# Kernel optimization log

Measured on AMD Instinct MI355X. Metric: run time of the kernel, lower is better.

Reference implementation:

```python
import jax, jax.numpy as jnp
import numpy as np

B, S, D, H, HD = 8, 1024, 1152, 16, 72
L, R = 32, 36  # get_decompose_dim(1152)
W_BITS, A_BITS = 4, 8


def _ste_round(x):
    return x + jax.lax.stop_gradient(jnp.round(x) - x)


def _fake_quant(x, bits):
    # symmetric fake quant, per last-dim group (per-token for acts, per-out-channel for weights)
    qmax = 2.0 ** (bits - 1) - 1.0
    scale = jnp.maximum(jnp.max(jnp.abs(x), axis=-1, keepdims=True) / qmax, 1e-8)
    return jnp.clip(_ste_round(x / scale), -qmax - 1.0, qmax) * scale


def _kron_apply(x, A, Bm):
    # DecomposeTransMatrix: x (..., L*R) -> reshape (L,R), Y = A^T X B (row-vector kron transform)
    sh = x.shape
    y = jnp.einsum('...lr,lp,rq->...pq', x.reshape(sh[:-1] + (L, R)), A, Bm)
    return y.reshape(sh)


def setup_inputs() -> dict:
    key = jax.random.key(0)
    ks = jax.random.split(key, 16)
    lin = lambda k, sh: jax.random.normal(k, sh, jnp.float32) * 0.02
    return {
        'hidden_states': jax.random.normal(ks[0], (B, S, D), jnp.float32),
        'Wq': lin(ks[1], (D, D)), 'bq': lin(ks[2], (D,)),
        'Wk': lin(ks[3], (D, D)), 'bk': lin(ks[4], (D,)),
        'Wv': lin(ks[5], (D, D)), 'bv': lin(ks[6], (D,)),
        'Wo': lin(ks[7], (D, D)), 'bo': lin(ks[8], (D,)),
        'ln_A': jnp.eye(L, dtype=jnp.float32) + 0.02 * jax.random.normal(ks[9], (L, L), jnp.float32),
        'ln_B': jnp.eye(R, dtype=jnp.float32) + 0.02 * jax.random.normal(ks[10], (R, R), jnp.float32),
        'ln_diag': 1.0 + 0.1 * jax.random.uniform(ks[11], (D,), jnp.float32),
        'vc': jnp.eye(HD, dtype=jnp.float32) + 0.02 * jax.random.normal(ks[12], (HD, HD), jnp.float32),
        'o_mat': jnp.eye(H, dtype=jnp.float32) + 0.02 * jax.random.normal(ks[13], (H, H), jnp.float32),
    }


def reference(hidden_states, Wq, bq, Wk, bk, Wv, bv, Wo, bo, ln_A, ln_B, ln_diag, vc, o_mat):
    invA_T = jnp.linalg.inv(ln_A).T
    invB_T = jnp.linalg.inv(ln_B).T
    # ln_trans applied to activations (diag scale + decomposed Kronecker rotation)
    x = _kron_apply(hidden_states * ln_diag, ln_A, ln_B)  # (B,S,D)

    def qlinear(xin, W, b, out_vc=None):
        # qa_trans inv_t folded into weight: W' = kron(W/diag, invA.T, invB.T) over input dim
        Wt = _kron_apply(W * (1.0 / ln_diag), invA_T, invB_T)
        bt = b
        if out_vc is not None:  # vc_trans folded into to_v output channels
            Wt = jnp.einsum('hdi,de->hei', Wt.reshape(H, HD, D), out_vc).reshape(D, D)
            bt = (b.reshape(H, HD) @ out_vc).reshape(-1)
        return _fake_quant(xin, A_BITS) @ _fake_quant(Wt, W_BITS).T + bt

    q = qlinear(x, Wq, bq).reshape(B, S, H, HD).transpose(0, 2, 1, 3)  # (B,H,S,HD)
    k = qlinear(x, Wk, bk).reshape(B, S, H, HD).transpose(0, 2, 1, 3)
    v = qlinear(x, Wv, bv, out_vc=vc).reshape(B, S, H, HD).transpose(0, 2, 1, 3)

    # baddbmm with beta=0, alpha=1: NO 1/sqrt(d) scaling (faithful to source)
    scores = jnp.einsum('bhqd,bhkd->bhqk', q, k)
    attn = jax.nn.softmax(scores.astype(jnp.float32), axis=-1).astype(q.dtype)
    ctx = jnp.einsum('bhqk,bhkd->bhqd', attn, v).transpose(0, 2, 1, 3)  # (B,S,H,HD)

    # o_trans: matmul(o_mat.T, Y) per token
    ctx = jnp.einsum('bsgd,gh->bshd', ctx, o_mat).reshape(B, S, D)

    # to_out with qa_trans=[inv(O).T, inv(V).T] folded into weight
    o_it = jnp.linalg.inv(o_mat).T
    v_it = jnp.linalg.inv(vc).T
    Wot = jnp.einsum('gh,ogd,de->ohe', o_it, Wo.reshape(D, H, HD), v_it).reshape(D, D)
    out = _fake_quant(ctx, A_BITS) @ _fake_quant(Wot, W_BITS).T + bo
    return out  # rescale_output_factor = 1.0
```

## Files before the change

kernel.cpp:

```cpp
#include <hip/hip_runtime.h>
#include <hip/hip_bf16.h>

#define BB 8
#define SS 1024
#define DD 1152
#define HH 16
#define HD 72
#define PD 96
#define LL 32
#define RR 36
#define NTOK (BB*SS)

typedef __attribute__((ext_vector_type(8)))  short short8;
typedef __attribute__((ext_vector_type(4)))  float f32x4;
typedef __attribute__((ext_vector_type(16))) float f32x16;
typedef __attribute__((ext_vector_type(4)))  unsigned short ushort4v;

#define F_IAT   0
#define F_IBT   1024
#define F_IO    2320
#define F_IV    2576
#define F_BVT   7760
#define F_SX    16384
#define F_SWQ   24576
#define F_SWK   25728
#define F_SWV   26880
#define F_SWO   28032
#define F_SCTX  32768
#define B_R1    1048576ULL
#define B_WB    (B_R1 + 37748736ULL)
#define B_XB    (B_WB + 4ULL*2654208ULL)
#define B_QB    (B_XB + 18874368ULL)
#define B_KB    (B_QB + 25165824ULL)
#define B_VB    (B_KB + 25165824ULL)
#define B_VT    (B_VB + 25165824ULL)
#define WSLOT   1327104ULL

__device__ __forceinline__ unsigned bf16rne(float f) {
    unsigned u = __builtin_bit_cast(unsigned, f);
    return (u + 0x7fffu + ((u >> 16) & 1u)) >> 16;
}
__device__ __forceinline__ unsigned cvtpk(float lo, float hi) {
    unsigned r;
    asm("v_cvt_pk_bf16_f32 %0, %1, %2" : "=v"(r) : "v"(lo), "v"(hi));
    return r;
}
__device__ __forceinline__ short8 mk8(unsigned a, unsigned b, unsigned c, unsigned d) {
    union { unsigned u[4]; short8 s; } t;
    t.u[0] = a; t.u[1] = b; t.u[2] = c; t.u[3] = d;
    return t.s;
}
__device__ __forceinline__ void async_ld16(void* lds, const void* g) {
    __builtin_amdgcn_global_load_lds((const __attribute__((address_space(1))) unsigned*)g,
                                     (__attribute__((address_space(3))) unsigned*)lds, 16, 0, 0);
}

__global__ __launch_bounds__(128) void invert_kernel(const float* __restrict__ A32, const float* __restrict__ B36,
                                                     const float* __restrict__ O16, const float* __restrict__ V72,
                                                     float* __restrict__ ws)
{
    __shared__ float As[80*76], Xs[80*76], Ys[80*76], Ps[80*76], Wt[80*76];
    int which = blockIdx.x;
    int n; const float* src;
    if (which == 0)      { n = 32; src = A32; }
    else if (which == 1) { n = 36; src = B36; }
    else if (which == 2) { n = 16; src = O16; }
    else                 { n = 72; src = V72; }
    int tid = threadIdx.x;
    int nq = n >> 2;
    for (int idx = tid; idx < n*n; idx += 128) {
        int i = idx / n, j = idx % n;
        float a = src[idx];
        As[i*76 + j] = a;
        Xs[i*76 + j] = (i == j ? 2.0f : 0.0f) - a;
    }
    __syncthreads();
    int ty = tid >> 3, qq = tid & 7;

#define NSGEMM(DST, SA, SB) { \
    f32x4 c00={0,0,0,0},c01={0,0,0,0},c02={0,0,0,0}, \
          c10={0,0,0,0},c11={0,0,0,0},c12={0,0,0,0}, \
          c20={0,0,0,0},c21={0,0,0,0},c22={0,0,0,0}, \
          c30={0,0,0,0},c31={0,0,0,0},c32={0,0,0,0}, \
          c40={0,0,0,0},c41={0,0,0,0},c42={0,0,0,0}; \
    _Pragma("unroll 2") \
    for (int k = 0; k < n; ++k) { \
        const float* sb = &SB[k*76]; \
        f32x4 b0 = *(const f32x4*)(sb + 4*qq); \
        f32x4 b1 = *(const f32x4*)(sb + 4*qq + 32); \
        f32x4 b2 = *(const f32x4*)(sb + 4*qq + 64); \
        float a0 = SA[ty*76 + k]; \
        float a1 = SA[(ty+16)*76 + k]; \
        float a2 = SA[(ty+32)*76 + k]; \
        float a3 = SA[(ty+48)*76 + k]; \
        float a4 = SA[(ty+64)*76 + k]; \
        c00 += a0*b0; c01 += a0*b1; c02 += a0*b2; \
        c10 += a1*b0; c11 += a1*b1; c12 += a1*b2; \
        c20 += a2*b0; c21 += a2*b1; c22 += a2*b2; \
        c30 += a3*b0; c31 += a3*b1; c32 += a3*b2; \
        c40 += a4*b0; c41 += a4*b1; c42 += a4*b2; \
    } \
    { \
        f32x4 cc[5][3] = {{c00,c01,c02},{c10,c11,c12},{c20,c21,c22},{c30,c31,c32},{c40,c41,c42}}; \
        _Pragma("unroll") \
        for (int m = 0; m < 5; ++m) { \
            int i = ty + 16*m; \
            if (i < n) { \
                _Pragma("unroll") \
                for (int c = 0; c < 3; ++c) { \
                    int q = qq + 8*c; \
                    if (q < nq) *(f32x4*)&DST[i*76 + 4*q] = cc[m][c]; \
                } \
            } \
        } \
    } \
}

#define NSELEM(PD_, YD_) { \
    for (int idx = tid; idx < n*n; idx += 128) { \
        int i = idx / n, j = idx % n; \
        PD_[i*76 + j] = PD_[i*76 + j] - 3.0f*YD_[i*76 + j] + (i == j ? 3.0f : 0.0f); \
    } \
}
    NSGEMM(Ys, As, Xs); __syncthreads();
    NSGEMM(Ps, Ys, Ys); __syncthreads();
    NSELEM(Ps, Ys);     __syncthreads();
    NSGEMM(Wt, Xs, Ps); __syncthreads();
    NSGEMM(Ys, As, Wt); __syncthreads();
    NSGEMM(Ps, Ys, Ys); __syncthreads();
    NSELEM(Ps, Ys);     __syncthreads();
    NSGEMM(Xs, Wt, Ps); __syncthreads();
#undef NSGEMM
#undef NSELEM

    if (which == 0) {
        for (int idx = tid; idx < 32*32; idx += 128) { int l = idx/32, pp = idx%32; ws[F_IAT + idx] = Xs[pp*76 + l]; }
    } else if (which == 1) {
        for (int idx = tid; idx < 36*36; idx += 128) { int r = idx/36, qx = idx%36; ws[F_IBT + idx] = Xs[qx*76 + r]; }
    } else if (which == 2) {
        for (int idx = tid; idx < 16*16; idx += 128) { int i = idx/16, j = idx%16; ws[F_IO + idx] = Xs[i*76 + j]; }
    } else {
        for (int idx = tid; idx < 72*72; idx += 128) { int i = idx/72, j = idx%72; ws[F_IV + idx] = Xs[i*76 + j]; }
    }
}

__global__ __launch_bounds__(256) void kron_act_q(const float* __restrict__ src, unsigned short* __restrict__ dst,
                                                  float* __restrict__ scl,
                                                  const float* __restrict__ P, const float* __restrict__ Q,
                                                  const float* __restrict__ diag)
{
    __shared__ float Xs[LL*RR], T1[LL*RR], Ps[LL*LL], Qs[RR*RR], Ys[LL*RR], red[256];
    int row = blockIdx.x;
    int tid = threadIdx.x;
    const float* sr = src + (size_t)row*DD;
    for (int i = tid; i < LL*LL; i += 256) Ps[i] = P[i];
    for (int i = tid; i < RR*RR; i += 256) Qs[i] = Q[i];
    for (int i = tid; i < DD; i += 256) Xs[i] = sr[i]*diag[i];
    __syncthreads();
    for (int s = tid; s < 288; s += 256) {
        int p = s / 9, r4 = (s % 9)*4;
        f32x4 acc = {0.f,0.f,0.f,0.f};
        #pragma unroll 8
        for (int l = 0; l < LL; ++l) {
            float a = Ps[l*LL + p];
            f32x4 x = *(const f32x4*)&Xs[l*RR + r4];
            acc += a*x;
        }
        *(f32x4*)&T1[p*RR + r4] = acc;
    }
    __syncthreads();
    float lmax = 0.f;
    for (int s = tid; s < 288; s += 256) {
        int p = s / 9, q4 = (s % 9)*4;
        f32x4 acc = {0.f,0.f,0.f,0.f};
        #pragma unroll 9
        for (int r = 0; r < RR; ++r) {
            float t = T1[p*RR + r];
            f32x4 qv = *(const f32x4*)&Qs[r*RR + q4];
            acc += t*qv;
        }
        *(f32x4*)&Ys[p*RR + q4] = acc;
        lmax = fmaxf(lmax, fmaxf(fmaxf(fabsf(acc[0]), fabsf(acc[1])), fmaxf(fabsf(acc[2]), fabsf(acc[3]))));
    }
    red[tid] = lmax; __syncthreads();
    for (int s = 128; s > 0; s >>= 1) { if (tid < s) red[tid] = fmaxf(red[tid], red[tid+s]); __syncthreads(); }
    float scale = fmaxf(red[0]/127.f, 1e-8f);
    float rs = 1.f/scale;
    if (tid == 0) scl[row] = scale;
    for (int s = tid; s < 288; s += 256) {
        int i4 = s*4;
        f32x4 y = *(const f32x4*)&Ys[i4];
        ushort4v o;
        #pragma unroll
        for (int c = 0; c < 4; ++c) {
            float v = rintf(y[c]*rs);
            v = fminf(fmaxf(v, -128.f), 127.f);
            o[c] = (unsigned short)bf16rne(v);
        }
        *(ushort4v*)&dst[(size_t)row*DD + i4] = o;
    }
}

__global__ __launch_bounds__(256) void kron_w_q(const float* __restrict__ src, unsigned short* __restrict__ dst,
                                                float* __restrict__ scl,
                                                const float* __restrict__ P, const float* __restrict__ Q,
                                                const float* __restrict__ diag)
{
    __shared__ float Xs[LL*RR], T1[LL*RR], Ps[LL*LL], Qs[RR*RR], Ys[LL*RR], red[256];
    int row = blockIdx.x;
    int tid = threadIdx.x;
    const float* sr = src + (size_t)row*DD;
    for (int i = tid; i < LL*LL; i += 256) Ps[i] = P[i];
    for (int i = tid; i < RR*RR; i += 256) Qs[i] = Q[i];
    for (int i = tid; i < DD; i += 256) Xs[i] = sr[i]*(1.0f/diag[i]);
    __syncthreads();
    for (int s = tid; s < 288; s += 256) {
        int p = s / 9, r4 = (s % 9)*4;
        f32x4 acc = {0.f,0.f,0.f,0.f};
        #pragma unroll 8
        for (int l = 0; l < LL; ++l) {
            float a = Ps[l*LL + p];
            f32x4 x = *(const f32x4*)&Xs[l*RR + r4];
            acc += a*x;
        }
        *(f32x4*)&T1[p*RR + r4] = acc;
    }
    __syncthreads();
    float lmax = 0.f;
    for (int s = tid; s < 288; s += 256) {
        int p = s / 9, q4 = (s % 9)*4;
        f32x4 acc = {0.f,0.f,0.f,0.f};
        #pragma unroll 9
        for (int r = 0; r < RR; ++r) {
            float t = T1[p*RR + r];
            f32x4 qv = *(const f32x4*)&Qs[r*RR + q4];
            acc += t*qv;
        }
        *(f32x4*)&Ys[p*RR + q4] = acc;
        lmax = fmaxf(lmax, fmaxf(fmaxf(fabsf(acc[0]), fabsf(acc[1])), fmaxf(fabsf(acc[2]), fabsf(acc[3]))));
    }
    red[tid] = lmax; __syncthreads();
    for (int s = 128; s > 0; s >>= 1) { if (tid < s) red[tid] = fmaxf(red[tid], red[tid+s]); __syncthreads(); }
    float scale = fmaxf(red[0]/7.f, 1e-8f);
    float rs = 1.f/scale;
    if (tid == 0) scl[row] = scale;
    for (int s = tid; s < 288; s += 256) {
        int i4 = s*4;
        f32x4 y = *(const f32x4*)&Ys[i4];
        ushort4v o;
        #pragma unroll
        for (int c = 0; c < 4; ++c) {
            float v = rintf(y[c]*rs);
            v = fminf(fmaxf(v, -8.f), 7.f);
            o[c] = (unsigned short)bf16rne(v);
        }
        *(ushort4v*)&dst[(size_t)row*DD + i4] = o;
    }
}

__global__ __launch_bounds__(256) void kron_rows(const float* __restrict__ src, float* __restrict__ dst,
                                                 const float* __restrict__ P, const float* __restrict__ Q,
                                                 const float* __restrict__ diag)
{
    __shared__ float Xs[LL*RR], T1[LL*RR], Ps[LL*LL], Qs[RR*RR];
    int row = blockIdx.x;
    int tid = threadIdx.x;
    const float* sr = src + (size_t)row*DD;
    for (int i = tid; i < LL*LL; i += 256) Ps[i] = P[i];
    for (int i = tid; i < RR*RR; i += 256) Qs[i] = Q[i];
    for (int i = tid; i < DD; i += 256) Xs[i] = sr[i]*(1.0f/diag[i]);
    __syncthreads();
    for (int s = tid; s < 288; s += 256) {
        int p = s / 9, r4 = (s % 9)*4;
        f32x4 acc = {0.f,0.f,0.f,0.f};
        #pragma unroll 8
        for (int l = 0; l < LL; ++l) {
            float a = Ps[l*LL + p];
            f32x4 x = *(const f32x4*)&Xs[l*RR + r4];
            acc += a*x;
        }
        *(f32x4*)&T1[p*RR + r4] = acc;
    }
    __syncthreads();
    for (int s = tid; s < 288; s += 256) {
        int p = s / 9, q4 = (s % 9)*4;
        f32x4 acc = {0.f,0.f,0.f,0.f};
        #pragma unroll 9
        for (int r = 0; r < RR; ++r) {
            float t = T1[p*RR + r];
            f32x4 qv = *(const f32x4*)&Qs[r*RR + q4];
            acc += t*qv;
        }
        *(f32x4*)&dst[(size_t)row*DD + p*RR + q4] = acc;
    }
}

__global__ __launch_bounds__(256) void wv_fold_q(const float* __restrict__ tmp, const float* __restrict__ vc,
                                                 const float* __restrict__ bv, unsigned short* __restrict__ dst,
                                                 float* __restrict__ scl, float* __restrict__ bvt)
{
    int he = blockIdx.x;
    int h = he / HD, e = he % HD;
    __shared__ float vcol[HD], Ys[DD], red[256];
    int tid = threadIdx.x;
    if (tid < HD) vcol[tid] = vc[tid*HD + e];
    __syncthreads();
    const float* base = tmp + (size_t)h*HD*DD;
    float lmax = 0.f;
    for (int i = tid; i < DD; i += 256) {
        float acc = 0.f;
        #pragma unroll 8
        for (int d = 0; d < HD; ++d) acc += base[(size_t)d*DD + i]*vcol[d];
        Ys[i] = acc;
        lmax = fmaxf(lmax, fabsf(acc));
    }
    red[tid] = lmax; __syncthreads();
    for (int s = 128; s > 0; s >>= 1) { if (tid < s) red[tid] = fmaxf(red[tid], red[tid+s]); __syncthreads(); }
    float scale = fmaxf(red[0]/7.f, 1e-8f);
    float rs = 1.f/scale;
    if (tid == 0) {
        scl[he] = scale;
        float acc = 0.f;
        for (int d = 0; d < HD; ++d) acc += bv[h*HD + d]*vcol[d];
        bvt[he] = acc;
    }
    for (int i = tid; i < DD; i += 256) {
        float v = rintf(Ys[i]*rs);
        v = fminf(fmaxf(v, -8.f), 7.f);
        dst[(size_t)he*DD + i] = (unsigned short)bf16rne(v);
    }
}

__global__ __launch_bounds__(256) void wo_trans_q(const float* __restrict__ Wo, const float* __restrict__ iO,
                                                  const float* __restrict__ iV, unsigned short* __restrict__ dst,
                                                  float* __restrict__ scl)
{
    __shared__ float M[HH*HD], T1[HH*HD], iOs[HH*HH], iVs[HD*HD], Ys[DD], red[256];
    int row = blockIdx.x, tid = threadIdx.x;
    for (int i = tid; i < DD; i += 256) M[i] = Wo[(size_t)row*DD + i];
    for (int i = tid; i < HH*HH; i += 256) iOs[i] = iO[i];
    for (int i = tid; i < HD*HD; i += 256) iVs[i] = iV[i];
    __syncthreads();
    for (int i = tid; i < DD; i += 256) {
        int h = i / HD, d = i % HD;
        float a = 0.f;
        #pragma unroll
        for (int g = 0; g < HH; ++g) a += iOs[h*HH + g]*M[g*HD + d];
        T1[i] = a;
    }
    __syncthreads();
    float lmax = 0.f;
    for (int i = tid; i < DD; i += 256) {
        int h = i / HD, e = i % HD;
        float a = 0.f;
        #pragma unroll 8
        for (int d = 0; d < HD; ++d) a += T1[h*HD + d]*iVs[e*HD + d];
        Ys[i] = a;
        lmax = fmaxf(lmax, fabsf(a));
    }
    red[tid] = lmax; __syncthreads();
    for (int s = 128; s > 0; s >>= 1) { if (tid < s) red[tid] = fmaxf(red[tid], red[tid+s]); __syncthreads(); }
    float scale = fmaxf(red[0]/7.f, 1e-8f);
    float rs = 1.f/scale;
    if (tid == 0) scl[row] = scale;
    for (int i = tid; i < DD; i += 256) {
        float v = rintf(Ys[i]*rs);
        v = fminf(fmaxf(v, -8.f), 7.f);
        dst[(size_t)row*DD + i] = (unsigned short)bf16rne(v);
    }
}

__device__ __forceinline__ void gemm_body(const unsigned short* __restrict__ Xb, const unsigned short* __restrict__ Wb,
                                          unsigned short* As, unsigned short* Bs, f32x4 (&acc)[4][4],
                                          int wr, int wc, int lr, int lg)
{
    for (int k0 = 0; k0 < DD; k0 += 32) {
        int tid = threadIdx.x;
        #pragma unroll
        for (int j = 0; j < 2; ++j) {
            int idx = tid + j*256;
            int row = idx >> 2, pp = idx & 3;
            int s = pp ^ ((row >> 1) & 3);
            async_ld16(&As[idx*8], Xb + (size_t)row*DD + k0 + s*8);
            async_ld16(&Bs[idx*8], Wb + (size_t)row*DD + k0 + s*8);
        }
        __syncthreads();
        short8 a[4], bfr[4];
        #pragma unroll
        for (int fr = 0; fr < 4; ++fr) {
            int row = wr*64 + fr*16 + lr;
            a[fr] = *(const short8*)(&As[row*32 + (lg ^ ((row>>1)&3))*8]);
        }
        #pragma unroll
        for (int fc = 0; fc < 4; ++fc) {
            int row = wc*64 + fc*16 + lr;
            bfr[fc] = *(const short8*)(&Bs[row*32 + (lg ^ ((row>>1)&3))*8]);
        }
        #pragma unroll
        for (int fr = 0; fr < 4; ++fr)
            #pragma unroll
            for (int fc = 0; fc < 4; ++fc)
                acc[fr][fc] = __builtin_amdgcn_mfma_f32_16x16x32_bf16(a[fr], bfr[fc], acc[fr][fc], 0, 0, 0);
        __syncthreads();
    }
}

__global__ __launch_bounds__(256) void gemm_qkv(const unsigned short* __restrict__ X,
                                                const unsigned short* __restrict__ Wq_b,
                                                const unsigned short* __restrict__ Wk_b,
                                                const unsigned short* __restrict__ Wv_b,
                                                const float* __restrict__ sx, const float* __restrict__ ws_all,
                                                const float* __restrict__ bq, const float* __restrict__ bk,
                                                const float* __restrict__ bvt,
                                                unsigned short* __restrict__ qb, unsigned short* __restrict__ kb,
                                                unsigned short* __restrict__ vb)
{
    __shared__ unsigned short As[128*32];
    __shared__ unsigned short Bs[128*32];
    int bn = blockIdx.x, bm = blockIdx.y, z = blockIdx.z;
    const unsigned short* W = (z == 0) ? Wq_b : (z == 1) ? Wk_b : Wv_b;
    const float* sw_ = ws_all + (size_t)z*1152;
    const float* bias = (z == 0) ? bq : (z == 1) ? bk : bvt;
    unsigned short* outQ = (z == 0) ? qb : (z == 1) ? kb : vb;
    int tid = threadIdx.x;
    if (bn == 0 && z <= 1) {
        short8 zero = {0,0,0,0,0,0,0,0};
        for (int t = tid; t < 6144; t += 256) {
            int tok = t / 48, rem = t % 48;
            int h = rem / 3, c = rem % 3;
            int mrow = bm*128 + tok;
            int b = mrow >> 10, s = mrow & 1023;
            *(short8*)(&outQ[(((size_t)b*HH + h)*SS + s)*PD + 72 + c*8]) = zero;
        }
    }
    int wave = tid >> 6, lane = tid & 63;
    int wr = wave >> 1, wc = wave & 1;
    int lr = lane & 15, lg = lane >> 4;
    f32x4 acc[4][4];
    #pragma unroll
    for (int i = 0; i < 4; ++i)
        #pragma unroll
        for (int j = 0; j < 4; ++j)
            #pragma unroll
            for (int e = 0; e < 4; ++e) acc[i][j][e] = 0.f;
    gemm_body(X + (size_t)bm*128*DD, W + (size_t)bn*128*DD, As, Bs, acc, wr, wc, lr, lg);
    #pragma unroll
    for (int fc = 0; fc < 4; ++fc) {
        int n = bn*128 + wc*64 + fc*16 + lr;
        float swn = sw_[n], bnv = bias[n];
        int h = n/72, hd = n - (n/72)*72;
        #pragma unroll
        for (int fr = 0; fr < 4; ++fr) {
            #pragma unroll
            for (int j = 0; j < 4; ++j) {
                int mrow = bm*128 + wr*64 + fr*16 + lg*4 + j;
                float v = acc[fr][fc][j]*sx[mrow]*swn + bnv;
                int b = mrow >> 10, s = mrow & 1023;
                outQ[(((size_t)b*HH + h)*SS + s)*PD + hd] = (unsigned short)bf16rne(v);
            }
        }
    }
}

__global__ __launch_bounds__(256) void gemm_out(const unsigned short* __restrict__ X, const unsigned short* __restrict__ W,
                                                const float* __restrict__ sx, const float* __restrict__ sw_,
                                                const float* __restrict__ bias, float* __restrict__ outF)
{
    __shared__ unsigned short As[128*32];
    __shared__ unsigned short Bs[128*32];
    int bn = blockIdx.x, bm = blockIdx.y;
    int tid = threadIdx.x;
    int wave = tid >> 6, lane = tid & 63;
    int wr = wave >> 1, wc = wave & 1;
    int lr = lane & 15, lg = lane >> 4;
    f32x4 acc[4][4];
    #pragma unroll
    for (int i = 0; i < 4; ++i)
        #pragma unroll
        for (int j = 0; j < 4; ++j)
            #pragma unroll
            for (int e = 0; e < 4; ++e) acc[i][j][e] = 0.f;
    gemm_body(X + (size_t)bm*128*DD, W + (size_t)bn*128*DD, As, Bs, acc, wr, wc, lr, lg);
    #pragma unroll
    for (int fc = 0; fc < 4; ++fc) {
        int n = bn*128 + wc*64 + fc*16 + lr;
        float swn = sw_[n], bnv = bias[n];
        #pragma unroll
        for (int fr = 0; fr < 4; ++fr) {
            #pragma unroll
            for (int j = 0; j < 4; ++j) {
                int mrow = bm*128 + wr*64 + fr*16 + lg*4 + j;
                outF[(size_t)mrow*DD + n] = acc[fr][fc][j]*sx[mrow]*swn + bnv;
            }
        }
    }
}

__global__ __launch_bounds__(256) void transpose_v(const unsigned short* __restrict__ v, unsigned short* __restrict__ vT)
{
    __shared__ unsigned short t[64][100];
    int head = blockIdx.x >> 4, st = blockIdx.x & 15;
    int tid = threadIdx.x;
    const unsigned short* src = v + ((size_t)head*SS + st*64)*PD;
    for (int idx = tid; idx < 64*PD; idx += 256) {
        int i = idx / PD, d = idx % PD;
        t[i][d] = src[idx];
    }
    __syncthreads();
    unsigned short* dst = vT + (size_t)head*PD*SS + st*64;
    for (int idx = tid; idx < PD*64; idx += 256) {
        int d = idx >> 6, i = idx & 63;
        dst[(size_t)d*SS + i] = t[i][d];
    }
}

__global__ __launch_bounds__(256) void attn_mfma(const unsigned short* __restrict__ q, const unsigned short* __restrict__ k,
                                                 const unsigned short* __restrict__ vT, float* __restrict__ ctx)
{
    __shared__ unsigned short Kl[64*128];
    __shared__ unsigned short Vl[96*64];
    int blk = blockIdx.x;
    int bh = blk >> 3;
    int qblk = blk & 7;
    int tid = threadIdx.x;
    int wave = tid >> 6, lane = tid & 63;
    int lq = lane & 31, half = lane >> 5;
    int b = bh >> 4, h = bh & 15;
    const unsigned short* qbase = q + ((size_t)bh*SS + qblk*128 + wave*32)*PD;
    const unsigned short* kbase = k + (size_t)bh*SS*PD;
    const unsigned short* vtb   = vT + (size_t)bh*PD*SS;
    short8 qf[6];
    #pragma unroll
    for (int ks = 0; ks < 6; ++ks)
        qf[ks] = *(const short8*)(qbase + (size_t)lq*PD + ks*16 + half*8);
    f32x16 O0, O1, O2;
    #pragma unroll
    for (int r = 0; r < 16; ++r) { O0[r] = 0.f; O1[r] = 0.f; O2[r] = 0.f; }
    float m = -1e30f, l = 0.f;
    for (int t0 = 0; t0 < SS; t0 += 64) {
        __syncthreads();
        #pragma unroll
        for (int j = 0; j < 3; ++j) {
            int idx = tid + j*256;
            int row = idx / 12, s = idx % 12;
            int phys = s ^ (row & 7);
            short8 val = *(const short8*)(kbase + (size_t)(t0 + row)*PD + s*8);
            *(short8*)(&Kl[row*128 + phys*8]) = val;
        }
        #pragma unroll
        for (int j = 0; j < 3; ++j) {
            int idx = tid + j*256;
            int d = idx >> 3, p = idx & 7;
            int s = p ^ (d & 7);
            short8 val = *(const short8*)(vtb + (size_t)d*SS + t0 + s*8);
            *(short8*)(&Vl[d*64 + p*8]) = val;
        }
        __syncthreads();
        #pragma unroll
        for (int sub = 0; sub < 2; ++sub) {
            f32x16 sacc;
            #pragma unroll
            for (int r = 0; r < 16; ++r) sacc[r] = 0.f;
            #pragma unroll
            for (int ks = 0; ks < 6; ++ks) {
                int key = sub*32 + lq;
                short8 kf = *(const short8*)(&Kl[key*128 + (((ks*2 + half) ^ (lq & 7)))*8]);
                sacc = __builtin_amdgcn_mfma_f32_32x32x16_bf16(kf, qf[ks], sacc, 0, 0, 0);
            }
            float pa = fmaxf(fmaxf(sacc[0], sacc[1]), fmaxf(sacc[2], sacc[3]));
            float pb = fmaxf(fmaxf(sacc[4], sacc[5]), fmaxf(sacc[6], sacc[7]));
            float pc = fmaxf(fmaxf(sacc[8], sacc[9]), fmaxf(sacc[10], sacc[11]));
            float pd = fmaxf(fmaxf(sacc[12], sacc[13]), fmaxf(sacc[14], sacc[15]));
            float pmax = fmaxf(fmaxf(pa, pb), fmaxf(pc, pd));
            pmax = fmaxf(pmax, __shfl_xor(pmax, 32));
            if (!__all(pmax - m <= 8.0f)) {
                float mn = fmaxf(m, pmax);
                float corr = __expf(m - mn);
                m = mn;
                l *= corr;
                #pragma unroll
                for (int r = 0; r < 16; ++r) {
                    int rowq = (r&3) + 8*(r>>2) + 4*half;
                    float cr = __shfl(corr, rowq);
                    O0[r] *= cr; O1[r] *= cr; O2[r] *= cr;
                }
            }
            float p[16]; float ls = 0.f;
            #pragma unroll
            for (int r = 0; r < 16; ++r) { p[r] = __expf(sacc[r] - m); ls += p[r]; }
            ls += __shfl_xor(ls, 32);
            l += ls;
            unsigned pk[8], sw[8];
            #pragma unroll
            for (int j2 = 0; j2 < 8; ++j2) pk[j2] = cvtpk(p[2*j2], p[2*j2+1]);
            #pragma unroll
            for (int j2 = 0; j2 < 8; ++j2) sw[j2] = __shfl_xor(pk[j2], 32);
            short8 A0 = half ? mk8(sw[2], sw[3], pk[2], pk[3]) : mk8(pk[0], pk[1], sw[0], sw[1]);
            short8 A1 = half ? mk8(sw[6], sw[7], pk[6], pk[7]) : mk8(pk[4], pk[5], sw[4], sw[5]);
            #pragma unroll
            for (int dt = 0; dt < 3; ++dt) {
                int d = dt*32 + lq;
                short8 vf0 = *(const short8*)(&Vl[d*64 + (((sub*4 + half) ^ (d & 7)))*8]);
                short8 vf1 = *(const short8*)(&Vl[d*64 + (((sub*4 + 2 + half) ^ (d & 7)))*8]);
                if (dt == 0) { O0 = __builtin_amdgcn_mfma_f32_32x32x16_bf16(A0, vf0, O0, 0,0,0);
                               O0 = __builtin_amdgcn_mfma_f32_32x32x16_bf16(A1, vf1, O0, 0,0,0); }
                if (dt == 1) { O1 = __builtin_amdgcn_mfma_f32_32x32x16_bf16(A0, vf0, O1, 0,0,0);
                               O1 = __builtin_amdgcn_mfma_f32_32x32x16_bf16(A1, vf1, O1, 0,0,0); }
                if (dt == 2) { O2 = __builtin_amdgcn_mfma_f32_32x32x16_bf16(A0, vf0, O2, 0,0,0);
                               O2 = __builtin_amdgcn_mfma_f32_32x32x16_bf16(A1, vf1, O2, 0,0,0); }
            }
        }
    }
    float linv = 1.f / l;
    #pragma unroll
    for (int r = 0; r < 16; ++r) {
        int rowq = (r&3) + 8*(r>>2) + 4*half;
        float lr = __shfl(linv, rowq);
        int s = qblk*128 + wave*32 + rowq;
        size_t base = ((size_t)(b*SS + s))*DD + h*HD;
        ctx[base + lq]      = O0[r]*lr;
        ctx[base + 32 + lq] = O1[r]*lr;
        if (lq < 8) ctx[base + 64 + lq] = O2[r]*lr;
    }
}

__global__ __launch_bounds__(256) void octx_fq_q(const float* __restrict__ ctx, const float* __restrict__ o_mat,
                                                 unsigned short* __restrict__ out, float* __restrict__ scl)
{
    __shared__ float ct[DD], Ys[DD], om[HH*HH], red[256];
    int t = blockIdx.x, tid = threadIdx.x;
    for (int i = tid; i < DD; i += 256) ct[i] = ctx[(size_t)t*DD + i];
    for (int i = tid; i < HH*HH; i += 256) om[i] = o_mat[i];
    __syncthreads();
    float lmax = 0.f;
    for (int s = tid; s < 288; s += 256) {
        int h = s / 18, d4 = (s % 18)*4;
        f32x4 acc = {0.f,0.f,0.f,0.f};
        #pragma unroll
        for (int g = 0; g < HH; ++g) {
            float o = om[g*HH + h];
            f32x4 c = *(const f32x4*)&ct[g*HD + d4];
            acc += o*c;
        }
        *(f32x4*)&Ys[h*HD + d4] = acc;
        lmax = fmaxf(lmax, fmaxf(fmaxf(fabsf(acc[0]), fabsf(acc[1])), fmaxf(fabsf(acc[2]), fabsf(acc[3]))));
    }
    red[tid] = lmax; __syncthreads();
    for (int s = 128; s > 0; s >>= 1) { if (tid < s) red[tid] = fmaxf(red[tid], red[tid+s]); __syncthreads(); }
    float scale = fmaxf(red[0]/127.f, 1e-8f);
    float rs = 1.f/scale;
    if (tid == 0) scl[t] = scale;
    for (int s = tid; s < 288; s += 256) {
        int i4 = s*4;
        f32x4 y = *(const f32x4*)&Ys[i4];
        ushort4v o;
        #pragma unroll
        for (int c = 0; c < 4; ++c) {
            float v = rintf(y[c]*rs);
            v = fminf(fmaxf(v, -128.f), 127.f);
            o[c] = (unsigned short)bf16rne(v);
        }
        *(ushort4v*)&out[(size_t)t*DD + i4] = o;
    }
}

extern "C" void kernel_launch(void* const* d_in, const int* in_sizes, int n_in,
                              void* d_out, int out_size, void* d_ws, size_t ws_size,
                              hipStream_t stream)
{
    const float* hidden = (const float*)d_in[0];
    const float* Wq = (const float*)d_in[1];  const float* bq = (const float*)d_in[2];
    const float* Wk = (const float*)d_in[3];  const float* bk = (const float*)d_in[4];
    const float* Wv = (const float*)d_in[5];  const float* bv = (const float*)d_in[6];
    const float* Wo = (const float*)d_in[7];  const float* bo = (const float*)d_in[8];
    const float* lnA = (const float*)d_in[9];
    const float* lnB = (const float*)d_in[10];
    const float* ln_diag = (const float*)d_in[11];
    const float* vc = (const float*)d_in[12];
    const float* o_mat = (const float*)d_in[13];
    float* ws = (float*)d_ws;
    float* out = (float*)d_out;
    char* wsb = (char*)d_ws;

    float* iAT  = ws + F_IAT;
    float* iBT  = ws + F_IBT;
    float* iO   = ws + F_IO;
    float* iV   = ws + F_IV;
    float* bvt  = ws + F_BVT;
    float* s_x  = ws + F_SX;
    float* s_wq = ws + F_SWQ;
    float* s_wk = ws + F_SWK;
    float* s_wv = ws + F_SWV;
    float* s_wo = ws + F_SWO;
    float* s_ct = ws + F_SCTX;

    float* slot = (float*)(wsb + B_R1);
    float* Wvm  = slot + 2*WSLOT;
    float* ctxf = slot;

    unsigned short* Wq_b = (unsigned short*)(wsb + B_WB);
    unsigned short* Wk_b = Wq_b + WSLOT;
    unsigned short* Wv_b = Wq_b + 2*WSLOT;
    unsigned short* Wo_b = Wq_b + 3*WSLOT;
    unsigned short* x_b  = (unsigned short*)(wsb + B_XB);
    unsigned short* ctx_b = x_b;
    unsigned short* qb = (unsigned short*)(wsb + B_QB);
    unsigned short* kb = (unsigned short*)(wsb + B_KB);
    unsigned short* vb = (unsigned short*)(wsb + B_VB);
    unsigned short* vT = (unsigned short*)(wsb + B_VT);

    invert_kernel<<<4, 128, 0, stream>>>(lnA, lnB, o_mat, vc, ws);
    kron_act_q<<<NTOK, 256, 0, stream>>>(hidden, x_b, s_x, lnA, lnB, ln_diag);
    kron_w_q<<<DD, 256, 0, stream>>>(Wq, Wq_b, s_wq, iAT, iBT, ln_diag);
    kron_w_q<<<DD, 256, 0, stream>>>(Wk, Wk_b, s_wk, iAT, iBT, ln_diag);
    kron_rows<<<DD, 256, 0, stream>>>(Wv, Wvm, iAT, iBT, ln_diag);
    wv_fold_q<<<DD, 256, 0, stream>>>(Wvm, vc, bv, Wv_b, s_wv, bvt);
    wo_trans_q<<<DD, 256, 0, stream>>>(Wo, iO, iV, Wo_b, s_wo);
    dim3 ggrid(DD/128, NTOK/128, 3);
    gemm_qkv<<<ggrid, 256, 0, stream>>>(x_b, Wq_b, Wk_b, Wv_b, s_x, s_wq, bq, bk, bvt, qb, kb, vb);
    transpose_v<<<BB*HH*16, 256, 0, stream>>>(vb, vT);
    attn_mfma<<<BB*HH*8, 256, 0, stream>>>(qb, kb, vT, ctxf);
    octx_fq_q<<<NTOK, 256, 0, stream>>>(ctxf, o_mat, ctx_b, s_ct);
    dim3 ogrid(DD/128, NTOK/128);
    gemm_out<<<ogrid, 256, 0, stream>>>(ctx_b, Wo_b, s_ct, s_wo, bo, out);
}
```

Before: 612.2 us.

## Store QKV token-major via LDS staging, remap blocks for XCDs, add MFMA priority

```diff
diff --git a/kernel.cpp b/kernel.cpp
--- a/kernel.cpp
+++ b/kernel.cpp
@@ -115,32 +115,31 @@
         } \
     } \
 }
-
-#define NSELEM(PD_, YD_) { \
+#define NSELEM(P_, Y_) { \
     for (int idx = tid; idx < n*n; idx += 128) { \
         int i = idx / n, j = idx % n; \
-        PD_[i*76 + j] = PD_[i*76 + j] - 3.0f*YD_[i*76 + j] + (i == j ? 3.0f : 0.0f); \
+        P_[i*76 + j] = P_[i*76 + j] - 3.0f*Y_[i*76 + j] + (i == j ? 3.0f : 0.0f); \
     } \
 }
-    NSGEMM(Ys, As, Xs); __syncthreads();
-    NSGEMM(Ps, Ys, Ys); __syncthreads();
-    NSELEM(Ps, Ys);     __syncthreads();
-    NSGEMM(Wt, Xs, Ps); __syncthreads();
-    NSGEMM(Ys, As, Wt); __syncthreads();
-    NSGEMM(Ps, Ys, Ys); __syncthreads();
-    NSELEM(Ps, Ys);     __syncthreads();
-    NSGEMM(Xs, Wt, Ps); __syncthreads();
+    float* Xc = Xs;
+    float* Xn = Wt;
+    for (int it = 0; it < 3; ++it) {
+        NSGEMM(Ys, As, Xc); __syncthreads();
+        NSGEMM(Ps, Ys, Ys); __syncthreads();
+        NSELEM(Ps, Ys);     __syncthreads();
+        NSGEMM(Xn, Xc, Ps); __syncthreads();
+        float* t = Xc; Xc = Xn; Xn = t;
+    }
 #undef NSGEMM
 #undef NSELEM
-
     if (which == 0) {
-        for (int idx = tid; idx < 32*32; idx += 128) { int l = idx/32, pp = idx%32; ws[F_IAT + idx] = Xs[pp*76 + l]; }
+        for (int idx = tid; idx < 32*32; idx += 128) { int l = idx/32, pp = idx%32; ws[F_IAT + idx] = Xc[pp*76 + l]; }
     } else if (which == 1) {
-        for (int idx = tid; idx < 36*36; idx += 128) { int r = idx/36, qx = idx%36; ws[F_IBT + idx] = Xs[qx*76 + r]; }
+        for (int idx = tid; idx < 36*36; idx += 128) { int r = idx/36, qx = idx%36; ws[F_IBT + idx] = Xc[qx*76 + r]; }
     } else if (which == 2) {
-        for (int idx = tid; idx < 16*16; idx += 128) { int i = idx/16, j = idx%16; ws[F_IO + idx] = Xs[i*76 + j]; }
+        for (int idx = tid; idx < 16*16; idx += 128) { int i = idx/16, j = idx%16; ws[F_IO + idx] = Xc[i*76 + j]; }
     } else {
-        for (int idx = tid; idx < 72*72; idx += 128) { int i = idx/72, j = idx%72; ws[F_IV + idx] = Xs[i*76 + j]; }
+        for (int idx = tid; idx < 72*72; idx += 128) { int i = idx/72, j = idx%72; ws[F_IV + idx] = Xc[i*76 + j]; }
     }
 }
 
@@ -415,24 +414,19 @@
                                                 unsigned short* __restrict__ qb, unsigned short* __restrict__ kb,
                                                 unsigned short* __restrict__ vb)
 {
-    __shared__ unsigned short As[128*32];
-    __shared__ unsigned short Bs[128*32];
-    int bn = blockIdx.x, bm = blockIdx.y, z = blockIdx.z;
+    __shared__ unsigned short smem[8192];
+    unsigned short* As = smem;
+    unsigned short* Bs = smem + 4096;
+    int lin = blockIdx.x;
+    int nl = (lin & 7)*216 + (lin >> 3);
+    int z = nl / 576;
+    int rem = nl - z*576;
+    int bm = rem / 9, bn = rem - bm*9;
     const unsigned short* W = (z == 0) ? Wq_b : (z == 1) ? Wk_b : Wv_b;
     const float* sw_ = ws_all + (size_t)z*1152;
     const float* bias = (z == 0) ? bq : (z == 1) ? bk : bvt;
     unsigned short* outQ = (z == 0) ? qb : (z == 1) ? kb : vb;
     int tid = threadIdx.x;
-    if (bn == 0 && z <= 1) {
-        short8 zero = {0,0,0,0,0,0,0,0};
-        for (int t = tid; t < 6144; t += 256) {
-            int tok = t / 48, rem = t % 48;
-            int h = rem / 3, c = rem % 3;
-            int mrow = bm*128 + tok;
-            int b = mrow >> 10, s = mrow & 1023;
-            *(short8*)(&outQ[(((size_t)b*HH + h)*SS + s)*PD + 72 + c*8]) = zero;
-        }
-    }
     int wave = tid >> 6, lane = tid & 63;
     int wr = wave >> 1, wc = wave & 1;
     int lr = lane & 15, lg = lane >> 4;
@@ -444,20 +438,38 @@
             #pragma unroll
             for (int e = 0; e < 4; ++e) acc[i][j][e] = 0.f;
     gemm_body(X + (size_t)bm*128*DD, W + (size_t)bn*128*DD, As, Bs, acc, wr, wc, lr, lg);
+    float swn[4], bnv[4];
     #pragma unroll
     for (int fc = 0; fc < 4; ++fc) {
         int n = bn*128 + wc*64 + fc*16 + lr;
-        float swn = sw_[n], bnv = bias[n];
-        int h = n/72, hd = n - (n/72)*72;
-        #pragma unroll
-        for (int fr = 0; fr < 4; ++fr) {
-            #pragma unroll
-            for (int j = 0; j < 4; ++j) {
-                int mrow = bm*128 + wr*64 + fr*16 + lg*4 + j;
-                float v = acc[fr][fc][j]*sx[mrow]*swn + bnv;
-                int b = mrow >> 10, s = mrow & 1023;
-                outQ[(((size_t)b*HH + h)*SS + s)*PD + hd] = (unsigned short)bf16rne(v);
+        swn[fc] = sw_[n]; bnv[fc] = bias[n];
+    }
+    #pragma unroll
+    for (int c = 0; c < 2; ++c) {
+        __syncthreads();
+        if (wr == c) {
+            #pragma unroll
+            for (int fr = 0; fr < 4; ++fr) {
+                #pragma unroll
+                for (int j = 0; j < 4; ++j) {
+                    int rloc = fr*16 + lg*4 + j;
+                    float sxm = sx[bm*128 + c*64 + rloc];
+                    #pragma unroll
+                    for (int fc = 0; fc < 4; ++fc) {
+                        int cloc = wc*64 + fc*16 + lr;
+                        float v = acc[fr][fc][j]*sxm*swn[fc] + bnv[fc];
+                        smem[rloc*128 + cloc] = (unsigned short)bf16rne(v);
+                    }
+                }
             }
+        }
+        __syncthreads();
+        #pragma unroll
+        for (int it = 0; it < 4; ++it) {
+            int idx = tid + it*256;
+            int row = idx >> 4, seg = idx & 15;
+            size_t g = ((size_t)(bm*128 + c*64 + row))*DD + bn*128 + seg*8;
+            *(short8*)(&outQ[g]) = *(const short8*)(&smem[row*128 + seg*8]);
         }
     }
 }
@@ -468,7 +480,9 @@
 {
     __shared__ unsigned short As[128*32];
     __shared__ unsigned short Bs[128*32];
-    int bn = blockIdx.x, bm = blockIdx.y;
+    int lin = blockIdx.x;
+    int nl = (lin & 7)*72 + (lin >> 3);
+    int bm = nl / 9, bn = nl - bm*9;
     int tid = threadIdx.x;
     int wave = tid >> 6, lane = tid & 63;
     int wr = wave >> 1, wc = wave & 1;
@@ -500,11 +514,12 @@
 {
     __shared__ unsigned short t[64][100];
     int head = blockIdx.x >> 4, st = blockIdx.x & 15;
-    int tid = threadIdx.x;
-    const unsigned short* src = v + ((size_t)head*SS + st*64)*PD;
+    int b = head >> 4, h = head & 15;
+    int tid = threadIdx.x;
+    const unsigned short* src = v + ((size_t)(b*SS + st*64))*DD + h*HD;
     for (int idx = tid; idx < 64*PD; idx += 256) {
         int i = idx / PD, d = idx % PD;
-        t[i][d] = src[idx];
+        t[i][d] = (d < HD) ? src[(size_t)i*DD + d] : (unsigned short)0;
     }
     __syncthreads();
     unsigned short* dst = vT + (size_t)head*PD*SS + st*64;
@@ -519,20 +534,24 @@
 {
     __shared__ unsigned short Kl[64*128];
     __shared__ unsigned short Vl[96*64];
-    int blk = blockIdx.x;
-    int bh = blk >> 3;
-    int qblk = blk & 7;
+    int lin = blockIdx.x;
+    int nl = (lin & 7)*128 + (lin >> 3);
+    int bh = nl >> 3;
+    int qblk = nl & 7;
     int tid = threadIdx.x;
     int wave = tid >> 6, lane = tid & 63;
     int lq = lane & 31, half = lane >> 5;
     int b = bh >> 4, h = bh & 15;
-    const unsigned short* qbase = q + ((size_t)bh*SS + qblk*128 + wave*32)*PD;
-    const unsigned short* kbase = k + (size_t)bh*SS*PD;
-    const unsigned short* vtb   = vT + (size_t)bh*PD*SS;
+    const unsigned short* qrow = q + ((size_t)(b*SS + qblk*128 + wave*32 + lq))*DD + h*HD;
+    const unsigned short* kbb  = k + (size_t)b*SS*DD + h*HD;
+    const unsigned short* vtb  = vT + (size_t)bh*PD*SS;
+    short8 zero8 = {0,0,0,0,0,0,0,0};
     short8 qf[6];
     #pragma unroll
-    for (int ks = 0; ks < 6; ++ks)
-        qf[ks] = *(const short8*)(qbase + (size_t)lq*PD + ks*16 + half*8);
+    for (int ks = 0; ks < 4; ++ks)
+        qf[ks] = *(const short8*)(qrow + ks*16 + half*8);
+    qf[4] = (half == 0) ? *(const short8*)(qrow + 64) : zero8;
+    qf[5] = zero8;
     f32x16 O0, O1, O2;
     #pragma unroll
     for (int r = 0; r < 16; ++r) { O0[r] = 0.f; O1[r] = 0.f; O2[r] = 0.f; }
@@ -544,7 +563,8 @@
             int idx = tid + j*256;
             int row = idx / 12, s = idx % 12;
             int phys = s ^ (row & 7);
-            short8 val = *(const short8*)(kbase + (size_t)(t0 + row)*PD + s*8);
+            short8 val = zero8;
+            if (s < 9) val = *(const short8*)(kbb + (size_t)(t0 + row)*DD + s*8);
             *(short8*)(&Kl[row*128 + phys*8]) = val;
         }
         #pragma unroll
@@ -561,12 +581,14 @@
             f32x16 sacc;
             #pragma unroll
             for (int r = 0; r < 16; ++r) sacc[r] = 0.f;
+            __builtin_amdgcn_s_setprio(1);
             #pragma unroll
             for (int ks = 0; ks < 6; ++ks) {
                 int key = sub*32 + lq;
                 short8 kf = *(const short8*)(&Kl[key*128 + (((ks*2 + half) ^ (lq & 7)))*8]);
                 sacc = __builtin_amdgcn_mfma_f32_32x32x16_bf16(kf, qf[ks], sacc, 0, 0, 0);
             }
+            __builtin_amdgcn_s_setprio(0);
             float pa = fmaxf(fmaxf(sacc[0], sacc[1]), fmaxf(sacc[2], sacc[3]));
             float pb = fmaxf(fmaxf(sacc[4], sacc[5]), fmaxf(sacc[6], sacc[7]));
             float pc = fmaxf(fmaxf(sacc[8], sacc[9]), fmaxf(sacc[10], sacc[11]));
@@ -597,6 +619,7 @@
             for (int j2 = 0; j2 < 8; ++j2) sw[j2] = __shfl_xor(pk[j2], 32);
             short8 A0 = half ? mk8(sw[2], sw[3], pk[2], pk[3]) : mk8(pk[0], pk[1], sw[0], sw[1]);
             short8 A1 = half ? mk8(sw[6], sw[7], pk[6], pk[7]) : mk8(pk[4], pk[5], sw[4], sw[5]);
+            __builtin_amdgcn_s_setprio(1);
             #pragma unroll
             for (int dt = 0; dt < 3; ++dt) {
                 int d = dt*32 + lq;
@@ -609,18 +632,19 @@
                 if (dt == 2) { O2 = __builtin_amdgcn_mfma_f32_32x32x16_bf16(A0, vf0, O2, 0,0,0);
                                O2 = __builtin_amdgcn_mfma_f32_32x32x16_bf16(A1, vf1, O2, 0,0,0); }
             }
+            __builtin_amdgcn_s_setprio(0);
         }
     }
     float linv = 1.f / l;
     #pragma unroll
     for (int r = 0; r < 16; ++r) {
         int rowq = (r&3) + 8*(r>>2) + 4*half;
-        float lr = __shfl(linv, rowq);
+        float lr2 = __shfl(linv, rowq);
         int s = qblk*128 + wave*32 + rowq;
         size_t base = ((size_t)(b*SS + s))*DD + h*HD;
-        ctx[base + lq]      = O0[r]*lr;
-        ctx[base + 32 + lq] = O1[r]*lr;
-        if (lq < 8) ctx[base + 64 + lq] = O2[r]*lr;
+        ctx[base + lq]      = O0[r]*lr2;
+        ctx[base + 32 + lq] = O1[r]*lr2;
+        if (lq < 8) ctx[base + 64 + lq] = O2[r]*lr2;
     }
 }
 
@@ -716,11 +740,9 @@
     kron_rows<<<DD, 256, 0, stream>>>(Wv, Wvm, iAT, iBT, ln_diag);
     wv_fold_q<<<DD, 256, 0, stream>>>(Wvm, vc, bv, Wv_b, s_wv, bvt);
     wo_trans_q<<<DD, 256, 0, stream>>>(Wo, iO, iV, Wo_b, s_wo);
-    dim3 ggrid(DD/128, NTOK/128, 3);
-    gemm_qkv<<<ggrid, 256, 0, stream>>>(x_b, Wq_b, Wk_b, Wv_b, s_x, s_wq, bq, bk, bvt, qb, kb, vb);
+    gemm_qkv<<<dim3(1728), 256, 0, stream>>>(x_b, Wq_b, Wk_b, Wv_b, s_x, s_wq, bq, bk, bvt, qb, kb, vb);
     transpose_v<<<BB*HH*16, 256, 0, stream>>>(vb, vT);
-    attn_mfma<<<BB*HH*8, 256, 0, stream>>>(qb, kb, vT, ctxf);
+    attn_mfma<<<dim3(1024), 256, 0, stream>>>(qb, kb, vT, ctxf);
     octx_fq_q<<<NTOK, 256, 0, stream>>>(ctxf, o_mat, ctx_b, s_ct);
-    dim3 ogrid(DD/128, NTOK/128);
-    gemm_out<<<ogrid, 256, 0, stream>>>(ctx_b, Wo_b, s_ct, s_wo, bo, out);
-}
+    gemm_out<<<dim3(576), 256, 0, stream>>>(ctx_b, Wo_b, s_ct, s_wo, bo, out);
+}
```

Result: no change. 620.5 us (+1.4%).
